# Performance work log

Hardware: AMD Instinct MI355X
Metric: run time of the kernel (lower is better)

## Reference

```python
import jax, jax.numpy as jnp
import numpy as np

B, C_IN, C_OUT = 4, 64, 64
Z = H = W = 64
MZ = MH = MW = 16
R = 16


def setup_inputs() -> dict:
    key = jax.random.key(0)
    ks = jax.random.split(key, 12)
    p = lambda k, s: jax.random.normal(k, s, jnp.float32) * 0.02
    return {
        "x": jax.random.normal(ks[0], (B, C_IN, Z, H, W), jnp.float32),
        "U_in": p(ks[1], (C_IN, R)),
        "U_out": p(ks[2], (C_OUT, R)),
        "U_z": p(ks[3], (MZ, R)),
        "U_h": p(ks[4], (MH, R)),
        "U_w": p(ks[5], (MW, R)),
        "U_z2": p(ks[6], (MZ, R)),
        "U_h2": p(ks[7], (MH, R)),
        "core_r": p(ks[8], (R, R, R, R, R)),
        "core_i": p(ks[9], (R, R, R, R, R)),
        "core2_r": p(ks[10], (R, R, R, R, R)),
        "core2_i": p(ks[11], (R, R, R, R, R)),
    }


def _reconstruct(U_in, U_out, Uz, Uh, Uw, core):
    # Original: einsum('ir,or,zr,hr,wr,abcde->iozwh', ..., core).
    # core's a..e indices are summed independently of the shared r index,
    # so the weight equals the CP outer product scaled by core.sum().
    c = jnp.complex64
    w = jnp.einsum('ir,or,zr,hr,wr->iozwh',
                   U_in.astype(c), U_out.astype(c), Uz.astype(c),
                   Uh.astype(c), Uw.astype(c))
    return w * jnp.sum(core)  # (in, out, mz, mw, mh)


def reference(x, U_in, U_out, U_z, U_h, U_w, U_z2, U_h2,
              core_r, core_i, core2_r, core2_i):
    mz, mh, mw = U_z.shape[0], U_h.shape[0], U_w.shape[0]
    b, _, z, h, w = x.shape
    core = core_r + 1j * core_i
    core2 = core2_r + 1j * core2_i

    x_ft = jnp.fft.rfftn(x, axes=(-3, -2, -1))  # (B, Cin, Z, H, W//2+1) c64
    w1 = _reconstruct(U_in, U_out, U_z, U_h, U_w, core)
    w2 = _reconstruct(U_in, U_out, U_z2, U_h2, U_w, core2)

    lo = jnp.einsum('bixyz,ioxyz->boxyz', x_ft[:, :, :mz, :mh, :mw], w1)
    hi = jnp.einsum('bixyz,ioxyz->boxyz', x_ft[:, :, -mz:, :mh, :mw], w2)

    out_ft = jnp.zeros((b, U_out.shape[0], z, h, w // 2 + 1), jnp.complex64)
    out_ft = out_ft.at[:, :, :mz, :mh, :mw].set(lo)
    out_ft = out_ft.at[:, :, -mz:, :mh, :mw].set(hi)

    return jnp.fft.irfftn(out_ft, s=(z, h, w), axes=(-3, -2, -1)).astype(jnp.float32)
```

## Files before the change

kernel.cpp:

```cpp
#include <hip/hip_runtime.h>

#define TWOPI 6.28318530717958647692f

constexpr float COSQ[17] = {
  1.0f, 0.995184727f, 0.980785280f, 0.956940336f, 0.923879533f,
  0.881921264f, 0.831469612f, 0.773010453f, 0.707106781f,
  0.634393284f, 0.555570233f, 0.471396737f, 0.382683432f,
  0.290284677f, 0.195090322f, 0.098017140f, 0.0f
};
__host__ __device__ constexpr float cos64f(int k) {
  k &= 63;
  return (k <= 16) ? COSQ[k] : (k < 32) ? -COSQ[32 - k]
       : (k <= 48) ? -COSQ[k - 32] : COSQ[64 - k];
}
__host__ __device__ constexpr float sin64f(int k) { return cos64f(k + 48); }


__global__ __launch_bounds__(256) void k_core_partial(
    const float* __restrict__ a0, const float* __restrict__ a1,
    const float* __restrict__ a2, const float* __restrict__ a3,
    float* __restrict__ partial) {
  const float* p = blockIdx.y == 0 ? a0 : blockIdx.y == 1 ? a1
                 : blockIdx.y == 2 ? a2 : a3;
  const float4* p4 = (const float4*)p;
  float s = 0.f;
  int base = blockIdx.x * 4096 + threadIdx.x;
  #pragma unroll
  for (int i = 0; i < 16; ++i) {
    float4 v = p4[base + i * 256];
    s += (v.x + v.y) + (v.z + v.w);
  }
  __shared__ float red[256];
  red[threadIdx.x] = s;
  __syncthreads();
  for (int off = 128; off; off >>= 1) {
    if (threadIdx.x < off) red[threadIdx.x] += red[threadIdx.x + off];
    __syncthreads();
  }
  if (threadIdx.x == 0) partial[blockIdx.y * 64 + blockIdx.x] = red[0];
}

__global__ void k_core_final(const float* __restrict__ partial,
                             float* __restrict__ S) {
  int t = threadIdx.x;
  if (t < 4) {
    float s = 0.f;
    for (int j = 0; j < 64; ++j) s += partial[t * 64 + j];
    S[t] = s;
  }
}

__global__ __launch_bounds__(256) void k_fwd_wh(const float* __restrict__ x,
                                                float2* __restrict__ A2) {
  __shared__ float2 T[4][64][17];
  int wave = threadIdx.x >> 6, lane = threadIdx.x & 63;
  int plane = blockIdx.x * 4 + wave;
  const float* xp = x + (size_t)plane * 4096 + lane;
  float cre[16], cim[16];
  {
    float x0 = xp[0], x32 = xp[32 * 64];
    #pragma unroll
    for (int hf = 0; hf < 16; ++hf) {
      cre[hf] = x0 + ((hf & 1) ? -x32 : x32);
      cim[hf] = 0.f;
    }
  }
  #pragma unroll
  for (int h = 1; h < 32; ++h) {
    float va = xp[h * 64], vb = xp[(64 - h) * 64];
    float u = va + vb, d = va - vb;
    #pragma unroll
    for (int hf = 0; hf < 16; ++hf) {
      cre[hf] = fmaf(u, cos64f(h * hf), cre[hf]);
      cim[hf] = fmaf(d, -sin64f(h * hf), cim[hf]);
    }
  }
  #pragma unroll
  for (int hf = 0; hf < 16; ++hf)
    T[wave][lane][hf] = make_float2(cre[hf], cim[hf]);
  __syncthreads();
  int hf = lane & 15, wq = lane >> 4;
  float2 rot[4], CS[4], acc[4];
  float2 T0 = T[wave][0][hf], T32 = T[wave][32][hf];
  #pragma unroll
  for (int j = 0; j < 4; ++j) {
    int wf = wq + 4 * j;
    float s, c;
    sincosf((TWOPI / 64.f) * (float)wf, &s, &c);
    rot[j] = make_float2(c, s);
    CS[j] = make_float2(c, s);
    float sgn = (wf & 1) ? -1.f : 1.f;
    acc[j] = make_float2(T0.x + sgn * T32.x, T0.y + sgn * T32.y);
  }
  #pragma unroll 4
  for (int w = 1; w < 32; ++w) {
    float2 a = T[wave][w][hf], b2 = T[wave][64 - w][hf];
    float Sr = a.x + b2.x, Si = a.y + b2.y;
    float Dr = a.x - b2.x, Di = a.y - b2.y;
    #pragma unroll
    for (int j = 0; j < 4; ++j) {
      float C = CS[j].x, Sn = CS[j].y;
      acc[j].x = fmaf(Sr, C, fmaf(Di, Sn, acc[j].x));
      acc[j].y = fmaf(Si, C, fmaf(-Dr, Sn, acc[j].y));
      float nC = C * rot[j].x - Sn * rot[j].y;
      CS[j].y = fmaf(C, rot[j].y, Sn * rot[j].x);
      CS[j].x = nC;
    }
  }
  float2* dst = A2 + (size_t)plane * 256 + lane;
  #pragma unroll
  for (int j = 0; j < 4; ++j) dst[j * 64] = acc[j];
}

__global__ __launch_bounds__(256) void k_proj(const float2* __restrict__ A2,
                                              float2* __restrict__ P,
                                              const float* __restrict__ U_in) {
  __shared__ float sU[1024];
  int t = threadIdx.x;
  #pragma unroll
  for (int i = 0; i < 4; ++i) sU[t + 256 * i] = U_in[t + 256 * i];
  __syncthreads();
  int b = blockIdx.x >> 6, z = blockIdx.x & 63;
  const float2* src = A2 + (((size_t)b * 64) * 64 + z) * 256 + t;
  float2 acc[16];
  #pragma unroll
  for (int r = 0; r < 16; ++r) acc[r] = make_float2(0.f, 0.f);
  for (int c = 0; c < 64; ++c) {
    float2 v = src[(size_t)c * 16384];
    #pragma unroll
    for (int r = 0; r < 16; ++r) {
      float u = sU[c * 16 + r];
      acc[r].x = fmaf(v.x, u, acc[r].x);
      acc[r].y = fmaf(v.y, u, acc[r].y);
    }
  }
  float2* dst = P + (((size_t)b * 16) * 64 + z) * 256 + t;
  #pragma unroll
  for (int r = 0; r < 16; ++r) dst[(size_t)r * 16384] = acc[r];
}

template <int KOFF>
__device__ __forceinline__ void fwd_z_body(const float2* __restrict__ src,
                                           float2* __restrict__ dst) {
  float2 acc[16];
  {
    float2 v0 = src[0], v32 = src[32 * 256];
    #pragma unroll
    for (int k = 0; k < 16; ++k) {
      float sgn = ((k + KOFF) & 1) ? -1.f : 1.f;
      acc[k] = make_float2(v0.x + sgn * v32.x, v0.y + sgn * v32.y);
    }
  }
  #pragma unroll
  for (int z = 1; z < 32; ++z) {
    float2 a = src[z * 256], b = src[(64 - z) * 256];
    float Sr = a.x + b.x, Si = a.y + b.y;
    float Dr = a.x - b.x, Di = a.y - b.y;
    #pragma unroll
    for (int k = 0; k < 16; ++k) {
      const float c = cos64f(z * (k + KOFF));
      const float s = sin64f(z * (k + KOFF));
      acc[k].x = fmaf(Sr, c, fmaf(Di, s, acc[k].x));
      acc[k].y = fmaf(Si, c, fmaf(-Dr, s, acc[k].y));
    }
  }
  #pragma unroll
  for (int k = 0; k < 16; ++k) dst[k * 256] = acc[k];
}

__global__ __launch_bounds__(256) void k_fwd_z2(const float2* __restrict__ P,
                                                float2* __restrict__ Pf) {
  int br = blockIdx.x, t = threadIdx.x;
  const float2* src = P + (size_t)br * 16384 + t;
  float2* dst = Pf + (size_t)br * 8192 + (size_t)blockIdx.y * 4096 + t;
  if (blockIdx.y == 0) fwd_z_body<0>(src, dst);
  else                 fwd_z_body<48>(src, dst);
}

template <int HALF>
__device__ __forceinline__ void inv_z_body(const float* __restrict__ gr,
                                           const float* __restrict__ gi,
                                           float2* __restrict__ dst) {
  if (HALF == 0) {
    {
      float sr = 0.f, si = 0.f;
      #pragma unroll
      for (int k = 0; k < 32; ++k) { sr += gr[k]; si += gi[k]; }
      dst[0] = make_float2(sr, si);
    }
    #pragma unroll
    for (int z = 1; z <= 16; ++z) {
      float Ar = 0.f, Ai = 0.f, Br = 0.f, Bi = 0.f;
      #pragma unroll
      for (int k = 0; k < 32; ++k) {
        const int f = (k < 16) ? k : (k + 32);
        const float c = cos64f(z * f), s = sin64f(z * f);
        Ar = fmaf(gr[k], c, Ar); Ai = fmaf(gi[k], c, Ai);
        Br = fmaf(gr[k], s, Br); Bi = fmaf(gi[k], s, Bi);
      }
      dst[z * 256] = make_float2(Ar - Bi, Ai + Br);
      dst[(64 - z) * 256] = make_float2(Ar + Bi, Ai - Br);
    }
  } else {
    {
      float sr = 0.f, si = 0.f;
      #pragma unroll
      for (int k = 0; k < 32; ++k) {
        if (k & 1) { sr -= gr[k]; si -= gi[k]; }
        else       { sr += gr[k]; si += gi[k]; }
      }
      dst[32 * 256] = make_float2(sr, si);
    }
    #pragma unroll
    for (int z = 17; z < 32; ++z) {
      float Ar = 0.f, Ai = 0.f, Br = 0.f, Bi = 0.f;
      #pragma unroll
      for (int k = 0; k < 32; ++k) {
        const int f = (k < 16) ? k : (k + 32);
        const float c = cos64f(z * f), s = sin64f(z * f);
        Ar = fmaf(gr[k], c, Ar); Ai = fmaf(gi[k], c, Ai);
        Br = fmaf(gr[k], s, Br); Bi = fmaf(gi[k], s, Bi);
      }
      dst[z * 256] = make_float2(Ar - Bi, Ai + Br);
      dst[(64 - z) * 256] = make_float2(Ar + Bi, Ai - Br);
    }
  }
}

__global__ __launch_bounds__(256) void k_scale_inv_z(
    const float2* __restrict__ Pf, float2* __restrict__ Q,
    const float* __restrict__ U_z, const float* __restrict__ U_h,
    const float* __restrict__ U_w, const float* __restrict__ U_z2,
    const float* __restrict__ U_h2, const float* __restrict__ S4) {
  int br = blockIdx.x, r = br & 15, t = threadIdx.x;
  int hf = t & 15, wf = ((t >> 4) & 3) + 4 * (t >> 6);
  const float2* src = Pf + (size_t)br * 8192 + t;
  const float invN = 1.0f / 262144.0f;
  float S1r = S4[0] * invN, S1i = S4[1] * invN;
  float S2r = S4[2] * invN, S2i = S4[3] * invN;
  float cw = U_w[hf * 16 + r];
  float ch1 = U_h[wf * 16 + r] * cw, ch2 = U_h2[wf * 16 + r] * cw;
  float gr[32], gi[32];
  #pragma unroll
  for (int k = 0; k < 16; ++k) {
    float2 v = src[k * 256];
    float g = U_z[k * 16 + r] * ch1;
    float Fr = S1r * g, Fi = S1i * g;
    gr[k] = v.x * Fr - v.y * Fi;
    gi[k] = v.x * Fi + v.y * Fr;
  }
  #pragma unroll
  for (int k = 0; k < 16; ++k) {
    float2 v = src[(k + 16) * 256];
    float g = U_z2[k * 16 + r] * ch2;
    float Fr = S2r * g, Fi = S2i * g;
    gr[k + 16] = v.x * Fr - v.y * Fi;
    gi[k + 16] = v.x * Fi + v.y * Fr;
  }
  float2* dst = Q + (size_t)br * 16384 + t;
  if (blockIdx.y == 0) inv_z_body<0>(gr, gi, dst);
  else                 inv_z_body<1>(gr, gi, dst);
}

__global__ __launch_bounds__(256) void k_expand_o(const float2* __restrict__ Q,
                                                  float2* __restrict__ Bz,
                                                  const float* __restrict__ U_out) {
  __shared__ float sU[1024];
  int t = threadIdx.x;
  #pragma unroll
  for (int i = 0; i < 4; ++i) sU[t + 256 * i] = U_out[t + 256 * i];
  __syncthreads();
  int b = blockIdx.x >> 6, z = blockIdx.x & 63;
  const float2* src = Q + (((size_t)b * 16) * 64 + z) * 256 + t;
  float2 q[16];
  #pragma unroll
  for (int r = 0; r < 16; ++r) q[r] = src[(size_t)r * 16384];
  float2* dst = Bz + (((size_t)b * 64) * 64 + z) * 256 + t;
  for (int o = 0; o < 64; ++o) {
    float re = 0.f, im = 0.f;
    #pragma unroll
    for (int r = 0; r < 16; ++r) {
      float u = sU[o * 16 + r];
      re = fmaf(q[r].x, u, re);
      im = fmaf(q[r].y, u, im);
    }
    dst[(size_t)o * 16384] = make_float2(re, im);
  }
}

__global__ __launch_bounds__(256) void k_inv_hw(const float2* __restrict__ Bz,
                                                float* __restrict__ out) {
  __shared__ float2 GL[4][256];
  int wave = threadIdx.x >> 6, lane = threadIdx.x & 63;
  int plane = blockIdx.x * 4 + wave;
  const float4* p4 = (const float4*)(Bz + (size_t)plane * 256);
  #pragma unroll
  for (int half = 0; half < 2; ++half) {
    float4 v = p4[lane + 64 * half];
    int t0 = 2 * (lane + 64 * half);
    int h0 = t0 & 15, w0 = ((t0 >> 4) & 3) + 4 * (t0 >> 6);
    int t1 = t0 + 1;
    int h1 = t1 & 15, w1 = ((t1 >> 4) & 3) + 4 * (t1 >> 6);
    GL[wave][h0 * 16 + w0] = make_float2(v.x, v.y);
    GL[wave][h1 * 16 + w1] = make_float2(v.z, v.w);
  }
  __syncthreads();
  float2 E2[16];
  {
    float s, c;
    sincosf((TWOPI / 64.f) * (float)lane, &s, &c);
    float2 E = make_float2(c, s);
    float2 St = E;
    #pragma unroll
    for (int wf = 1; wf < 16; ++wf) {
      E2[wf] = make_float2(E.x + E.x, E.y + E.y);
      float ex = E.x * St.x - E.y * St.y;
      E.y = fmaf(E.x, St.y, E.y * St.x);
      E.x = ex;
    }
  }
  float qre[16], qim[16];
  #pragma unroll
  for (int hf = 0; hf < 16; ++hf) {
    const float2* gp = &GL[wave][hf * 16];
    float2 g0 = gp[0], g1 = gp[1];
    float ar = g0.x + (g1.x * E2[1].x - g1.y * E2[1].y);
    float ai = g0.y + (g1.x * E2[1].y + g1.y * E2[1].x);
    #pragma unroll
    for (int wf = 2; wf < 16; ++wf) {
      float2 gv = gp[wf];
      ar = fmaf(gv.x, E2[wf].x, fmaf(-gv.y, E2[wf].y, ar));
      ai = fmaf(gv.x, E2[wf].y, fmaf(gv.y, E2[wf].x, ai));
    }
    qre[hf] = ar; qim[hf] = ai;
  }
  float* op = out + (size_t)plane * 4096 + lane;
  {
    float P = qre[0];
    #pragma unroll
    for (int hf = 1; hf < 16; ++hf) P += qre[hf];
    op[0] = P;
  }
  {
    float P = qre[0];
    #pragma unroll
    for (int hf = 1; hf < 16; ++hf) P += (hf & 1) ? -qre[hf] : qre[hf];
    op[32 * 64] = P;
  }
  #pragma unroll
  for (int h = 1; h < 32; ++h) {
    float P = qre[0], Q = 0.f;
    #pragma unroll
    for (int hf = 1; hf < 16; ++hf) {
      P = fmaf(qre[hf], cos64f(h * hf), P);
      Q = fmaf(qim[hf], sin64f(h * hf), Q);
    }
    op[h * 64] = P - Q;
    op[(64 - h) * 64] = P + Q;
  }
}

extern "C" void kernel_launch(void* const* d_in, const int* in_sizes, int n_in,
                              void* d_out, int out_size, void* d_ws,
                              size_t ws_size, hipStream_t stream) {
  const float* x    = (const float*)d_in[0];
  const float* Uin  = (const float*)d_in[1];
  const float* Uout = (const float*)d_in[2];
  const float* Uz   = (const float*)d_in[3];
  const float* Uh   = (const float*)d_in[4];
  const float* Uw   = (const float*)d_in[5];
  const float* Uz2  = (const float*)d_in[6];
  const float* Uh2  = (const float*)d_in[7];
  const float* cr   = (const float*)d_in[8];
  const float* ci   = (const float*)d_in[9];
  const float* c2r  = (const float*)d_in[10];
  const float* c2i  = (const float*)d_in[11];
  float* outp = (float*)d_out;

  char* ws = (char*)d_ws;
  float* S       = (float*)ws;
  float* partial = (float*)(ws + 256);
  float2* A2 = (float2*)(ws + 4096);
  float2* P  = (float2*)(ws + 33558528);
  float2* Pf = (float2*)(ws + 41947136);
  float2* Q  = (float2*)(ws + 50335744);
  float2* Bz = A2;

  k_core_partial<<<dim3(64, 4), 256, 0, stream>>>(cr, ci, c2r, c2i, partial);
  k_core_final<<<1, 64, 0, stream>>>(partial, S);
  k_fwd_wh<<<4096, 256, 0, stream>>>(x, A2);
  k_proj<<<256, 256, 0, stream>>>(A2, P, Uin);
  k_fwd_z2<<<dim3(64, 2), 256, 0, stream>>>(P, Pf);
  k_scale_inv_z<<<dim3(64, 2), 256, 0, stream>>>(Pf, Q, Uz, Uh, Uw, Uz2, Uh2,
                                                 S);
  k_expand_o<<<256, 256, 0, stream>>>(Q, Bz, Uout);
  k_inv_hw<<<4096, 256, 0, stream>>>(Bz, outp);
}
```

Measured before the change: 206.3 us.

## Fuse output-channel expansion into inverse HW DFT and merge z-DFT stages

Fuses the U_out channel expansion directly into the inverse H/W DFT kernel so the large intermediate Bz buffer is never written to or read from global memory. It also merges the forward z DFT into the scale/inverse-z kernel and folds the core-sum finalization into k_proj, reducing the launch count. The trade-off is fewer blocks with heavier per-block work and larger LDS usage in the fused inverse kernel, plus redundant forward-z computation across the two halves.

```diff
diff --git a/kernel.cpp b/kernel.cpp
--- a/kernel.cpp
+++ b/kernel.cpp
@@ -40,16 +40,6 @@
   if (threadIdx.x == 0) partial[blockIdx.y * 64 + blockIdx.x] = red[0];
 }
 
-__global__ void k_core_final(const float* __restrict__ partial,
-                             float* __restrict__ S) {
-  int t = threadIdx.x;
-  if (t < 4) {
-    float s = 0.f;
-    for (int j = 0; j < 64; ++j) s += partial[t * 64 + j];
-    S[t] = s;
-  }
-}
-
 __global__ __launch_bounds__(256) void k_fwd_wh(const float* __restrict__ x,
                                                 float2* __restrict__ A2) {
   __shared__ float2 T[4][64][17];
@@ -114,7 +104,14 @@
 
 __global__ __launch_bounds__(256) void k_proj(const float2* __restrict__ A2,
                                               float2* __restrict__ P,
-                                              const float* __restrict__ U_in) {
+                                              const float* __restrict__ U_in,
+                                              const float* __restrict__ partial,
+                                              float* __restrict__ S) {
+  if (blockIdx.x == 0 && threadIdx.x < 4) {
+    float s = 0.f;
+    for (int j = 0; j < 64; ++j) s += partial[threadIdx.x * 64 + j];
+    S[threadIdx.x] = s;
+  }
   __shared__ float sU[1024];
   int t = threadIdx.x;
   #pragma unroll
@@ -137,44 +134,6 @@
   float2* dst = P + (((size_t)b * 16) * 64 + z) * 256 + t;
   #pragma unroll
   for (int r = 0; r < 16; ++r) dst[(size_t)r * 16384] = acc[r];
-}
-
-template <int KOFF>
-__device__ __forceinline__ void fwd_z_body(const float2* __restrict__ src,
-                                           float2* __restrict__ dst) {
-  float2 acc[16];
-  {
-    float2 v0 = src[0], v32 = src[32 * 256];
-    #pragma unroll
-    for (int k = 0; k < 16; ++k) {
-      float sgn = ((k + KOFF) & 1) ? -1.f : 1.f;
-      acc[k] = make_float2(v0.x + sgn * v32.x, v0.y + sgn * v32.y);
-    }
-  }
-  #pragma unroll
-  for (int z = 1; z < 32; ++z) {
-    float2 a = src[z * 256], b = src[(64 - z) * 256];
-    float Sr = a.x + b.x, Si = a.y + b.y;
-    float Dr = a.x - b.x, Di = a.y - b.y;
-    #pragma unroll
-    for (int k = 0; k < 16; ++k) {
-      const float c = cos64f(z * (k + KOFF));
-      const float s = sin64f(z * (k + KOFF));
-      acc[k].x = fmaf(Sr, c, fmaf(Di, s, acc[k].x));
-      acc[k].y = fmaf(Si, c, fmaf(-Dr, s, acc[k].y));
-    }
-  }
-  #pragma unroll
-  for (int k = 0; k < 16; ++k) dst[k * 256] = acc[k];
-}
-
-__global__ __launch_bounds__(256) void k_fwd_z2(const float2* __restrict__ P,
-                                                float2* __restrict__ Pf) {
-  int br = blockIdx.x, t = threadIdx.x;
-  const float2* src = P + (size_t)br * 16384 + t;
-  float2* dst = Pf + (size_t)br * 8192 + (size_t)blockIdx.y * 4096 + t;
-  if (blockIdx.y == 0) fwd_z_body<0>(src, dst);
-  else                 fwd_z_body<48>(src, dst);
 }
 
 template <int HALF>
@@ -227,14 +186,44 @@
   }
 }
 
-__global__ __launch_bounds__(256) void k_scale_inv_z(
-    const float2* __restrict__ Pf, float2* __restrict__ Q,
+__global__ __launch_bounds__(256) void k_zmix(
+    const float2* __restrict__ P, float2* __restrict__ Q,
     const float* __restrict__ U_z, const float* __restrict__ U_h,
     const float* __restrict__ U_w, const float* __restrict__ U_z2,
     const float* __restrict__ U_h2, const float* __restrict__ S4) {
   int br = blockIdx.x, r = br & 15, t = threadIdx.x;
   int hf = t & 15, wf = ((t >> 4) & 3) + 4 * (t >> 6);
-  const float2* src = Pf + (size_t)br * 8192 + t;
+  const float2* src = P + (size_t)br * 16384 + t;
+  float2 acc[32];
+  {
+    float2 v0 = src[0], v32 = src[32 * 256];
+    #pragma unroll
+    for (int k = 0; k < 16; ++k) {
+      float sgn = (k & 1) ? -1.f : 1.f;
+      float2 e = make_float2(v0.x + sgn * v32.x, v0.y + sgn * v32.y);
+      acc[k] = e;
+      acc[k + 16] = e;
+    }
+  }
+  #pragma unroll
+  for (int z = 1; z < 32; ++z) {
+    float2 a = src[z * 256], b = src[(64 - z) * 256];
+    float Sr = a.x + b.x, Si = a.y + b.y;
+    float Dr = a.x - b.x, Di = a.y - b.y;
+    #pragma unroll
+    for (int k = 0; k < 16; ++k) {
+      {
+        const float c = cos64f(z * k), s = sin64f(z * k);
+        acc[k].x = fmaf(Sr, c, fmaf(Di, s, acc[k].x));
+        acc[k].y = fmaf(Si, c, fmaf(-Dr, s, acc[k].y));
+      }
+      {
+        const float c = cos64f(z * (k + 48)), s = sin64f(z * (k + 48));
+        acc[k + 16].x = fmaf(Sr, c, fmaf(Di, s, acc[k + 16].x));
+        acc[k + 16].y = fmaf(Si, c, fmaf(-Dr, s, acc[k + 16].y));
+      }
+    }
+  }
   const float invN = 1.0f / 262144.0f;
   float S1r = S4[0] * invN, S1i = S4[1] * invN;
   float S2r = S4[2] * invN, S2i = S4[3] * invN;
@@ -243,7 +232,7 @@
   float gr[32], gi[32];
   #pragma unroll
   for (int k = 0; k < 16; ++k) {
-    float2 v = src[k * 256];
+    float2 v = acc[k];
     float g = U_z[k * 16 + r] * ch1;
     float Fr = S1r * g, Fi = S1i * g;
     gr[k] = v.x * Fr - v.y * Fi;
@@ -251,7 +240,7 @@
   }
   #pragma unroll
   for (int k = 0; k < 16; ++k) {
-    float2 v = src[(k + 16) * 256];
+    float2 v = acc[k + 16];
     float g = U_z2[k * 16 + r] * ch2;
     float Fr = S2r * g, Fi = S2i * g;
     gr[k + 16] = v.x * Fr - v.y * Fi;
@@ -262,49 +251,21 @@
   else                 inv_z_body<1>(gr, gi, dst);
 }
 
-__global__ __launch_bounds__(256) void k_expand_o(const float2* __restrict__ Q,
-                                                  float2* __restrict__ Bz,
-                                                  const float* __restrict__ U_out) {
+__global__ __launch_bounds__(256) void k_inv_hw_ex(
+    const float2* __restrict__ Q, float* __restrict__ out,
+    const float* __restrict__ U_out) {
+  __shared__ float2 sQ[16][256];
+  __shared__ float2 GLo[4][256];
   __shared__ float sU[1024];
   int t = threadIdx.x;
+  int b = blockIdx.x >> 6, z = blockIdx.x & 63, og = blockIdx.y;
   #pragma unroll
   for (int i = 0; i < 4; ++i) sU[t + 256 * i] = U_out[t + 256 * i];
+  #pragma unroll
+  for (int r = 0; r < 16; ++r)
+    sQ[r][t] = Q[((size_t)(b * 16 + r) * 64 + z) * 256 + t];
   __syncthreads();
-  int b = blockIdx.x >> 6, z = blockIdx.x & 63;
-  const float2* src = Q + (((size_t)b * 16) * 64 + z) * 256 + t;
-  float2 q[16];
-  #pragma unroll
-  for (int r = 0; r < 16; ++r) q[r] = src[(size_t)r * 16384];
-  float2* dst = Bz + (((size_t)b * 64) * 64 + z) * 256 + t;
-  for (int o = 0; o < 64; ++o) {
-    float re = 0.f, im = 0.f;
-    #pragma unroll
-    for (int r = 0; r < 16; ++r) {
-      float u = sU[o * 16 + r];
-      re = fmaf(q[r].x, u, re);
-      im = fmaf(q[r].y, u, im);
-    }
-    dst[(size_t)o * 16384] = make_float2(re, im);
-  }
-}
-
-__global__ __launch_bounds__(256) void k_inv_hw(const float2* __restrict__ Bz,
-                                                float* __restrict__ out) {
-  __shared__ float2 GL[4][256];
-  int wave = threadIdx.x >> 6, lane = threadIdx.x & 63;
-  int plane = blockIdx.x * 4 + wave;
-  const float4* p4 = (const float4*)(Bz + (size_t)plane * 256);
-  #pragma unroll
-  for (int half = 0; half < 2; ++half) {
-    float4 v = p4[lane + 64 * half];
-    int t0 = 2 * (lane + 64 * half);
-    int h0 = t0 & 15, w0 = ((t0 >> 4) & 3) + 4 * (t0 >> 6);
-    int t1 = t0 + 1;
-    int h1 = t1 & 15, w1 = ((t1 >> 4) & 3) + 4 * (t1 >> 6);
-    GL[wave][h0 * 16 + w0] = make_float2(v.x, v.y);
-    GL[wave][h1 * 16 + w1] = make_float2(v.z, v.w);
-  }
-  __syncthreads();
+  int wave = t >> 6, lane = t & 63;
   float2 E2[16];
   {
     float s, c;
@@ -312,51 +273,66 @@
     float2 E = make_float2(c, s);
     float2 St = E;
     #pragma unroll
-    for (int wf = 1; wf < 16; ++wf) {
-      E2[wf] = make_float2(E.x + E.x, E.y + E.y);
+    for (int wfi = 1; wfi < 16; ++wfi) {
+      E2[wfi] = make_float2(E.x + E.x, E.y + E.y);
       float ex = E.x * St.x - E.y * St.y;
       E.y = fmaf(E.x, St.y, E.y * St.x);
       E.x = ex;
     }
   }
-  float qre[16], qim[16];
-  #pragma unroll
-  for (int hf = 0; hf < 16; ++hf) {
-    const float2* gp = &GL[wave][hf * 16];
-    float2 g0 = gp[0], g1 = gp[1];
-    float ar = g0.x + (g1.x * E2[1].x - g1.y * E2[1].y);
-    float ai = g0.y + (g1.x * E2[1].y + g1.y * E2[1].x);
-    #pragma unroll
-    for (int wf = 2; wf < 16; ++wf) {
-      float2 gv = gp[wf];
-      ar = fmaf(gv.x, E2[wf].x, fmaf(-gv.y, E2[wf].y, ar));
-      ai = fmaf(gv.x, E2[wf].y, fmaf(gv.y, E2[wf].x, ai));
-    }
-    qre[hf] = ar; qim[hf] = ai;
-  }
-  float* op = out + (size_t)plane * 4096 + lane;
-  {
-    float P = qre[0];
-    #pragma unroll
-    for (int hf = 1; hf < 16; ++hf) P += qre[hf];
-    op[0] = P;
-  }
-  {
-    float P = qre[0];
-    #pragma unroll
-    for (int hf = 1; hf < 16; ++hf) P += (hf & 1) ? -qre[hf] : qre[hf];
-    op[32 * 64] = P;
-  }
-  #pragma unroll
-  for (int h = 1; h < 32; ++h) {
-    float P = qre[0], Q = 0.f;
-    #pragma unroll
-    for (int hf = 1; hf < 16; ++hf) {
-      P = fmaf(qre[hf], cos64f(h * hf), P);
-      Q = fmaf(qim[hf], sin64f(h * hf), Q);
-    }
-    op[h * 64] = P - Q;
-    op[(64 - h) * 64] = P + Q;
+  for (int oi = 0; oi < 8; ++oi) {
+    int o = og * 32 + wave * 8 + oi;
+    #pragma unroll
+    for (int q = 0; q < 4; ++q) {
+      int tt = lane + 64 * q;
+      float re = 0.f, im = 0.f;
+      #pragma unroll
+      for (int r = 0; r < 16; ++r) {
+        float u = sU[o * 16 + r];
+        float2 v = sQ[r][tt];
+        re = fmaf(v.x, u, re);
+        im = fmaf(v.y, u, im);
+      }
+      GLo[wave][tt] = make_float2(re, im);
+    }
+    float qre[16], qim[16];
+    #pragma unroll
+    for (int hfi = 0; hfi < 16; ++hfi) {
+      float2 g0 = GLo[wave][hfi];
+      float ar = g0.x, ai = g0.y;
+      #pragma unroll
+      for (int wfi = 1; wfi < 16; ++wfi) {
+        float2 gv = GLo[wave][(wfi >> 2) * 64 + (wfi & 3) * 16 + hfi];
+        ar = fmaf(gv.x, E2[wfi].x, fmaf(-gv.y, E2[wfi].y, ar));
+        ai = fmaf(gv.x, E2[wfi].y, fmaf(gv.y, E2[wfi].x, ai));
+      }
+      qre[hfi] = ar; qim[hfi] = ai;
+    }
+    float* op = out + (((size_t)(b * 64 + o) * 64 + z)) * 4096 + lane;
+    {
+      float Pv = qre[0];
+      #pragma unroll
+      for (int hfi = 1; hfi < 16; ++hfi) Pv += qre[hfi];
+      op[0] = Pv;
+    }
+    {
+      float Pv = qre[0];
+      #pragma unroll
+      for (int hfi = 1; hfi < 16; ++hfi)
+        Pv += (hfi & 1) ? -qre[hfi] : qre[hfi];
+      op[32 * 64] = Pv;
+    }
+    #pragma unroll
+    for (int h = 1; h < 32; ++h) {
+      float Pv = qre[0], Qv = 0.f;
+      #pragma unroll
+      for (int hfi = 1; hfi < 16; ++hfi) {
+        Pv = fmaf(qre[hfi], cos64f(h * hfi), Pv);
+        Qv = fmaf(qim[hfi], sin64f(h * hfi), Qv);
+      }
+      op[h * 64] = Pv - Qv;
+      op[(64 - h) * 64] = Pv + Qv;
+    }
   }
 }
 
@@ -382,17 +358,11 @@
   float* partial = (float*)(ws + 256);
   float2* A2 = (float2*)(ws + 4096);
   float2* P  = (float2*)(ws + 33558528);
-  float2* Pf = (float2*)(ws + 41947136);
-  float2* Q  = (float2*)(ws + 50335744);
-  float2* Bz = A2;
+  float2* Q  = (float2*)(ws + 41947136);
 
   k_core_partial<<<dim3(64, 4), 256, 0, stream>>>(cr, ci, c2r, c2i, partial);
-  k_core_final<<<1, 64, 0, stream>>>(partial, S);
   k_fwd_wh<<<4096, 256, 0, stream>>>(x, A2);
-  k_proj<<<256, 256, 0, stream>>>(A2, P, Uin);
-  k_fwd_z2<<<dim3(64, 2), 256, 0, stream>>>(P, Pf);
-  k_scale_inv_z<<<dim3(64, 2), 256, 0, stream>>>(Pf, Q, Uz, Uh, Uw, Uz2, Uh2,
-                                                 S);
-  k_expand_o<<<256, 256, 0, stream>>>(Q, Bz, Uout);
-  k_inv_hw<<<4096, 256, 0, stream>>>(Bz, outp);
-}
+  k_proj<<<256, 256, 0, stream>>>(A2, P, Uin, partial, S);
+  k_zmix<<<dim3(64, 2), 256, 0, stream>>>(P, Q, Uz, Uh, Uw, Uz2, Uh2, S);
+  k_inv_hw_ex<<<dim3(256, 2), 256, 0, stream>>>(Q, outp, Uout);
+}
```

After: 194.4 us. 5.8% less time.
